# Kernel optimization log

Measured on AMD Instinct MI355X. Metric: run time of the kernel, lower is better.

The kernel has to match this reference:

```python
import jax, jax.numpy as jnp
import numpy as np

N_NODES = 100000
N_EDGES = 1000000
N_INPUT = 64
N_HIDDEN = 64
K = 8


def setup_inputs() -> dict:
    key = jax.random.key(0)
    k1, k2, k3, k4 = jax.random.split(key, 4)
    x = jax.random.normal(k1, (N_NODES, N_INPUT), dtype=jnp.float32)
    edge_index = jax.random.randint(k2, (2, N_EDGES), 0, N_NODES, dtype=jnp.int64)
    # ChebConv has K independent [in, out] weight matrices (Glorot-ish scale) and a bias.
    weight = jax.random.normal(k3, (K, N_INPUT, N_HIDDEN), dtype=jnp.float32) * (1.0 / np.sqrt(N_INPUT))
    bias = jax.random.normal(k4, (N_HIDDEN,), dtype=jnp.float32) * 0.01
    return {"x": x, "edge_index": edge_index, "weight": weight, "bias": bias}


def _cheb_edge_norm(edge_index, num_nodes):
    # PyG ChebConv sym normalization with default lambda_max=2.0:
    #   L_hat = (2/lambda_max) * (I - D^-1/2 A D^-1/2) - I = -D^-1/2 A D^-1/2
    # (the diagonal +1 from the Laplacian and the -1 self-loop cancel exactly).
    src, dst = edge_index[0], edge_index[1]
    ones = jnp.ones(src.shape[0], dtype=jnp.float32)
    deg = jax.ops.segment_sum(ones, src, num_segments=num_nodes)
    deg_inv_sqrt = jnp.where(deg > 0, jax.lax.rsqrt(jnp.maximum(deg, 1.0)), 0.0)
    return -deg_inv_sqrt[src] * deg_inv_sqrt[dst]  # [E]


def reference(x, edge_index, weight, bias):
    num_nodes = x.shape[0]
    src, dst = edge_index[0], edge_index[1]
    norm = _cheb_edge_norm(edge_index, num_nodes)

    def prop(h):  # h: [N, F] -> L_hat @ h via gather-multiply-scatter over edges
        return jax.ops.segment_sum(norm[:, None] * h[src], dst, num_segments=num_nodes)

    # Chebyshev recursion: T0 = x, T1 = L_hat x, Tk = 2 L_hat T_{k-1} - T_{k-2}
    Tx0 = x
    out = Tx0 @ weight[0]
    Tx1 = prop(Tx0)
    out = out + Tx1 @ weight[1]
    for k in range(2, weight.shape[0]):
        Tx2 = 2.0 * prop(Tx1) - Tx0
        out = out + Tx2 @ weight[k]
        Tx0, Tx1 = Tx1, Tx2
    out = out + bias
    # bn=False path: ReLU then dropout (identity in eval mode)
    return jax.nn.relu(out)
```

## Files before the change

### kernel.cpp

```cpp
#include <hip/hip_runtime.h>
#include <hip/hip_bf16.h>

typedef __attribute__((ext_vector_type(8))) short s16x8;
typedef __attribute__((ext_vector_type(4))) float f32x4;

#define HC 48
#define RBH 6400
#define RBS 3200

static __device__ __forceinline__ unsigned short f2bf(float f) {
    unsigned int u = __float_as_uint(f);
    unsigned int r = (u + 0x7FFFu + ((u >> 16) & 1u)) >> 16;
    return (unsigned short)r;
}

__global__ __launch_bounds__(256) void k_hist(const int* __restrict__ eidx,
                                              unsigned short* __restrict__ partials,
                                              int N, int E, int HR) {
    __shared__ int h[RBH];
    int b = blockIdx.x;
    int job = b / (HR * HC);
    int rc = b % (HR * HC);
    int r = rc / HC, c = rc % HC;
    int lo = r * RBH;
    int nb = min(RBH, N - lo);
    if (nb <= 0) return;
    for (int i = threadIdx.x; i < nb; i += 256) h[i] = 0;
    __syncthreads();
    const int* vals = eidx + (size_t)job * E;
    int e0 = (int)(((long long)E * c / HC) & ~3LL);
    int e1 = (c == HC - 1) ? E : (int)(((long long)E * (c + 1) / HC) & ~3LL);
    int e = e0 + threadIdx.x * 4;
    for (; e + 4 <= e1; e += 1024) {
        int4 v = *reinterpret_cast<const int4*>(vals + e);
        unsigned r0 = (unsigned)(v.x - lo), r1 = (unsigned)(v.y - lo);
        unsigned r2 = (unsigned)(v.z - lo), r3 = (unsigned)(v.w - lo);
        if (r0 < (unsigned)nb) atomicAdd(&h[r0], 1);
        if (r1 < (unsigned)nb) atomicAdd(&h[r1], 1);
        if (r2 < (unsigned)nb) atomicAdd(&h[r2], 1);
        if (r3 < (unsigned)nb) atomicAdd(&h[r3], 1);
    }
    if (threadIdx.x == 0)
        for (int t = e1 & ~3; t < e1; ++t) {
            unsigned rel = (unsigned)(vals[t] - lo);
            if (rel < (unsigned)nb) atomicAdd(&h[rel], 1);
        }
    __syncthreads();
    unsigned short* outp = partials + ((size_t)(job * HC + c)) * N + lo;
    for (int i = threadIdx.x; i < nb; i += 256) outp[i] = (unsigned short)h[i];
}

__global__ __launch_bounds__(1024) void k_rs(const unsigned short* __restrict__ partials,
                                             float* __restrict__ dis,
                                             float* __restrict__ dsi,
                                             int* __restrict__ cnt,
                                             int* __restrict__ incl,
                                             int* __restrict__ bsum, int N) {
    __shared__ int sm[1024];
    int t = threadIdx.x;
    int i = blockIdx.x * 1024 + t;
    int csum = 0;
    if (i < N) {
        int dsum = 0;
        for (int c = 0; c < HC; ++c) {
            dsum += partials[(size_t)c * N + i];
            csum += partials[(size_t)(HC + c) * N + i];
        }
        dis[i] = dsum > 0 ? rsqrtf((float)dsum) : 0.f;
        dsi[i] = dsum > 0 ? sqrtf((float)dsum) : 0.f;
        cnt[i] = csum;
    }
    sm[t] = (i < N) ? csum : 0;
    __syncthreads();
    for (int off = 1; off < 1024; off <<= 1) {
        int add = (t >= off) ? sm[t - off] : 0;
        __syncthreads();
        sm[t] += add;
        __syncthreads();
    }
    if (i < N) incl[i] = sm[t];
    if (t == 1023) bsum[blockIdx.x] = sm[1023];
}

__global__ __launch_bounds__(1024) void k_scan3(const int* __restrict__ cnt,
                                                const int* __restrict__ bsum,
                                                int* __restrict__ rowptr,
                                                const unsigned short* __restrict__ pdst,
                                                int* __restrict__ cbase, int N, int nb) {
    __shared__ int sb[128];
    int t = threadIdx.x;
    if (t < 128) sb[t] = (t < nb) ? bsum[t] : 0;
    __syncthreads();
    for (int off = 1; off < 128; off <<= 1) {
        int add = (t < 128 && t >= off) ? sb[t - off] : 0;
        __syncthreads();
        if (t < 128) sb[t] += add;
        __syncthreads();
    }
    int b = blockIdx.x;
    int boff = (b == 0) ? 0 : sb[b - 1];
    int total = sb[nb - 1];
    int i = b * 1024 + t;
    if (i >= N) return;
    int ex = rowptr[i] - cnt[i] + boff;
    rowptr[i] = ex;
    if (i == N - 1) rowptr[N] = total;
    int run = ex;
    for (int c = 0; c < HC; ++c) {
        size_t idx = (size_t)c * N + i;
        cbase[idx] = run;
        run += pdst[idx];
    }
}

__global__ __launch_bounds__(256) void k_scatter(
        const int* __restrict__ src, const int* __restrict__ dst,
        const int* __restrict__ cbase, int* __restrict__ srcs, int N, int E) {
    __shared__ int cur[RBS];
    int r = blockIdx.x / HC, c = blockIdx.x % HC;
    int lo = r * RBS;
    int nb = min(RBS, N - lo);
    if (nb <= 0) return;
    for (int i = threadIdx.x; i < nb; i += 256)
        cur[i] = cbase[(size_t)c * N + lo + i];
    __syncthreads();
    int e0 = (int)(((long long)E * c / HC) & ~3LL);
    int e1 = (c == HC - 1) ? E : (int)(((long long)E * (c + 1) / HC) & ~3LL);
    int e = e0 + threadIdx.x * 4;
    for (; e + 4 <= e1; e += 1024) {
        int4 d4 = *reinterpret_cast<const int4*>(dst + e);
        unsigned r0 = (unsigned)(d4.x - lo), r1 = (unsigned)(d4.y - lo);
        unsigned r2 = (unsigned)(d4.z - lo), r3 = (unsigned)(d4.w - lo);
        if (r0 < (unsigned)nb) srcs[atomicAdd(&cur[r0], 1)] = src[e];
        if (r1 < (unsigned)nb) srcs[atomicAdd(&cur[r1], 1)] = src[e + 1];
        if (r2 < (unsigned)nb) srcs[atomicAdd(&cur[r2], 1)] = src[e + 2];
        if (r3 < (unsigned)nb) srcs[atomicAdd(&cur[r3], 1)] = src[e + 3];
    }
    if (threadIdx.x == 0)
        for (int t = e1 & ~3; t < e1; ++t) {
            unsigned rel = (unsigned)(dst[t] - lo);
            if (rel < (unsigned)nb) srcs[atomicAdd(&cur[rel], 1)] = src[t];
        }
}

__global__ void k_pack(const float* __restrict__ x, const float* __restrict__ dis,
                       const float* __restrict__ W,
                       unsigned short* __restrict__ ysb, unsigned short* __restrict__ wt,
                       float* __restrict__ walt,
                       int N, int K, int PSE) {
    int t = blockIdx.x * blockDim.x + threadIdx.x;
    int nys = (N + 1) * 32;
    if (t < nys) {
        int row = t >> 5, p = t & 31;
        if (row == N) {
            for (int k = 0; k < K; ++k)
                *(unsigned*)(ysb + (size_t)k * PSE + ((size_t)N << 6) + (p << 1)) = 0;
            return;
        }
        size_t o = ((size_t)row << 6) + (p << 1);
        float2 v = *reinterpret_cast<const float2*>(x + o);
        float dv = dis[row];
        *(unsigned*)(ysb + o) = (unsigned)f2bf(v.x * dv) | ((unsigned)f2bf(v.y * dv) << 16);
    } else {
        int u = t - nys;
        if (u < K * 4096) {
            float v = W[u];
            int k = u >> 12;
            int r = u & 4095;
            int i = r >> 6;
            int j = r & 63;
            wt[(size_t)j * (K * 64) + (k << 6) + i] = f2bf(v);
        } else if (u < K * 4096 + 4096) {
            int u2 = u - K * 4096;
            float s = 0.f;
            for (int k = 0; k < K; k += 2)
                s += ((k & 3) == 0 ? 1.f : -1.f) * W[k * 4096 + u2];
            walt[u2] = s;
        }
    }
}

static __device__ __forceinline__ void addrow(float* acc, uint4 t) {
    acc[0] += __uint_as_float(t.x << 16);
    acc[1] += __uint_as_float(t.x & 0xffff0000u);
    acc[2] += __uint_as_float(t.y << 16);
    acc[3] += __uint_as_float(t.y & 0xffff0000u);
    acc[4] += __uint_as_float(t.z << 16);
    acc[5] += __uint_as_float(t.z & 0xffff0000u);
    acc[6] += __uint_as_float(t.w << 16);
    acc[7] += __uint_as_float(t.w & 0xffff0000u);
}

__global__ __launch_bounds__(256) void k_prop(
        const unsigned short* __restrict__ Ysin,
        const unsigned short* __restrict__ Ysm2,
        unsigned short* __restrict__ Ysout,
        const int* __restrict__ rowptr, const int* __restrict__ srcs,
        const float* __restrict__ dis,
        int N, int E, float scale, float beta) {
    int gt = blockIdx.x * blockDim.x + threadIdx.x;
    int wave0 = (gt >> 6) << 3;
    int lane = gt & 63;
    int g = lane >> 3;
    int i = lane & 7;
    int node = wave0 + g;
    bool live = node < N;
    int rs = 0, deg = 0;
    if (live) {
        rs = rowptr[node];
        deg = rowptr[node + 1] - rs;
    }
    int wmax = deg;
#pragma unroll
    for (int m = 8; m <= 32; m <<= 1) {
        int o = __shfl_xor(wmax, m);
        wmax = o > wmax ? o : wmax;
    }
    float acc[8];
#pragma unroll
    for (int j = 0; j < 8; ++j) acc[j] = 0.f;
    for (int e = 0; e < wmax; e += 8) {
        int b = rs + e;
        int s[8];
#pragma unroll
        for (int q = 0; q < 8; ++q)
            s[q] = (e + q < deg) ? srcs[min(b + q, E - 1)] : N;
        uint4 t[8];
#pragma unroll
        for (int q = 0; q < 8; ++q)
            t[q] = *reinterpret_cast<const uint4*>(Ysin + ((size_t)s[q] << 6) + (i << 3));
#pragma unroll
        for (int q = 0; q < 8; ++q) addrow(acc, t[q]);
    }
    if (live) {
        float dv = dis[node];
        float sc = -scale * dv * dv;
        size_t base = ((size_t)node << 6) + (i << 3);
        float r[8];
#pragma unroll
        for (int j = 0; j < 8; ++j) r[j] = sc * acc[j];
        if (beta != 0.f) {
            uint4 pv = *reinterpret_cast<const uint4*>(Ysm2 + base);
            r[0] = fmaf(beta, __uint_as_float(pv.x << 16), r[0]);
            r[1] = fmaf(beta, __uint_as_float(pv.x & 0xffff0000u), r[1]);
            r[2] = fmaf(beta, __uint_as_float(pv.y << 16), r[2]);
            r[3] = fmaf(beta, __uint_as_float(pv.y & 0xffff0000u), r[3]);
            r[4] = fmaf(beta, __uint_as_float(pv.z << 16), r[4]);
            r[5] = fmaf(beta, __uint_as_float(pv.z & 0xffff0000u), r[5]);
            r[6] = fmaf(beta, __uint_as_float(pv.w << 16), r[6]);
            r[7] = fmaf(beta, __uint_as_float(pv.w & 0xffff0000u), r[7]);
        }
        uint4 ov;
        ov.x = (unsigned)f2bf(r[0]) | ((unsigned)f2bf(r[1]) << 16);
        ov.y = (unsigned)f2bf(r[2]) | ((unsigned)f2bf(r[3]) << 16);
        ov.z = (unsigned)f2bf(r[4]) | ((unsigned)f2bf(r[5]) << 16);
        ov.w = (unsigned)f2bf(r[6]) | ((unsigned)f2bf(r[7]) << 16);
        *reinterpret_cast<uint4*>(Ysout + base) = ov;
    }
}

template <int KS>
__global__ __launch_bounds__(256) void k_gemm(const unsigned short* __restrict__ tb,
                                              const unsigned short* __restrict__ wt,
                                              const float* __restrict__ bias,
                                              const float* __restrict__ dsi,
                                              const float* __restrict__ x,
                                              const float* __restrict__ walt,
                                              float* __restrict__ out,
                                              int N, int PSE) {
    constexpr int NB = KS / 2;
    __shared__ unsigned short lds_b[KS * 512];
    __shared__ unsigned short lds_a[KS * 256 * 8];
    int tid = threadIdx.x;
    int lane = tid & 63;
    int w = tid >> 6;
    int l16 = lane & 15;
    int quad = lane >> 4;
    const int KI = KS * 32;

    {
        const unsigned short* wrow = wt + (size_t)(w * 16 + l16) * KI + quad * 8;
#pragma unroll
        for (int ks = 0; ks < KS; ++ks) {
            s16x8 v = *reinterpret_cast<const s16x8*>(wrow + ks * 32);
            *reinterpret_cast<s16x8*>(lds_a + (ks * 256 + tid) * 8) = v;
        }
    }
    f32x4 bias4 = *reinterpret_cast<const f32x4*>(bias + w * 16 + quad * 4);

    int ntiles = N >> 4;
    for (int t = blockIdx.x; t < ntiles; t += gridDim.x) {
        const char* tilebase = (const char*)tb + (size_t)t * 2048;
#pragma unroll
        for (int inst = 0; inst < 2 * NB; ++inst) {
            if ((inst & 3) != w) continue;
            int kbuf = inst >> 1;
            int j = inst & 1;
            int p = j * 64 + lane;
            int nrow = p >> 3;
            int s = (p & 7) ^ (nrow & 7);
            const char* g = tilebase + (size_t)kbuf * PSE * 2 + nrow * 128 + s * 16;
            __builtin_amdgcn_global_load_lds(
                (const __attribute__((address_space(1))) unsigned int*)g,
                (__attribute__((address_space(3))) unsigned int*)(lds_b + inst * 512),
                16, 0, 0);
        }
        __syncthreads();
        f32x4 acc = {0.f, 0.f, 0.f, 0.f};
#pragma unroll
        for (int ks = 0; ks < KS; ++ks) {
            s16x8 af = *reinterpret_cast<const s16x8*>(lds_a + (ks * 256 + tid) * 8);
            int kbuf = ks >> 1, half = ks & 1;
            int sph = (half * 4 + quad) ^ (l16 & 7);
            s16x8 bf = *reinterpret_cast<const s16x8*>(
                lds_b + kbuf * 1024 + l16 * 64 + sph * 8);
            acc = __builtin_amdgcn_mfma_f32_16x16x32_bf16(af, bf, acc, 0, 0, 0);
        }
        int row = t * 16 + l16;
        float dvi = dsi[row];
        float* orow = out + (size_t)row * 64 + w * 16 + quad * 4;
        f32x4 r;
        if (dvi != 0.f) {
#pragma unroll
            for (int q = 0; q < 4; ++q) {
                float v = fmaf(acc[q], dvi, bias4[q]);
                r[q] = v > 0.f ? v : 0.f;
            }
        } else {
            const float* xr = x + (size_t)row * 64;
            float rr[4] = {bias4[0], bias4[1], bias4[2], bias4[3]};
            for (int j = 0; j < 64; ++j) {
                float xv = xr[j];
                const float* wr = walt + j * 64 + w * 16 + quad * 4;
#pragma unroll
                for (int q = 0; q < 4; ++q) rr[q] = fmaf(xv, wr[q], rr[q]);
            }
#pragma unroll
            for (int q = 0; q < 4; ++q) r[q] = rr[q] > 0.f ? rr[q] : 0.f;
        }
        *reinterpret_cast<f32x4*>(orow) = r;
        __syncthreads();
    }
}

extern "C" void kernel_launch(void* const* d_in, const int* in_sizes, int n_in,
                              void* d_out, int out_size, void* d_ws, size_t ws_size,
                              hipStream_t stream) {
    const float* x    = (const float*)d_in[0];
    const int*   eidx = (const int*)d_in[1];
    const float* W    = (const float*)d_in[2];
    const float* bias = (const float*)d_in[3];
    float* out = (float*)d_out;

    const int NF = in_sizes[0];
    const int N  = NF / 64;
    const int E  = in_sizes[1] / 2;
    const int K  = in_sizes[2] / 4096;

    const int* src = eidx;
    const int* dst = eidx + E;

    const int PSE = (N + 1) * 64;

    char* ws = (char*)d_ws;
    size_t off = 0;
    auto alloc = [&](size_t bytes) -> char* {
        char* p = ws + off;
        off = (off + bytes + 255) & ~(size_t)255;
        return p;
    };
    unsigned short* Ysb = (unsigned short*)alloc((size_t)K * PSE * 2);
    unsigned short* Wt = (unsigned short*)alloc((size_t)64 * K * 64 * 2);
    float* Walt  = (float*)alloc(4096 * 4);
    int*   srcs   = (int*)alloc((size_t)E * 4);
    int*   rowptr = (int*)alloc((size_t)(N + 1) * 4);
    int*   cnt    = (int*)alloc((size_t)N * 4);
    unsigned short* partials = (unsigned short*)alloc((size_t)2 * HC * N * 2);
    int*   cbase  = (int*)alloc((size_t)HC * N * 4);
    float* dis  = (float*)alloc((size_t)N * 4);
    float* dsi  = (float*)alloc((size_t)N * 4);
    int*   bsum = (int*)alloc(1024);
    (void)ws_size; (void)n_in; (void)out_size;

    int HR = (N + RBH - 1) / RBH;
    int SR = (N + RBS - 1) / RBS;
    const unsigned short* pdst = partials + (size_t)HC * N;

    k_hist<<<2 * HR * HC, 256, 0, stream>>>(eidx, partials, N, E, HR);
    int nb = (N + 1023) / 1024;
    k_rs<<<nb, 1024, 0, stream>>>(partials, dis, dsi, cnt, rowptr, bsum, N);
    k_scan3<<<nb, 1024, 0, stream>>>(cnt, bsum, rowptr, pdst, cbase, N, nb);
    k_scatter<<<SR * HC, 256, 0, stream>>>(src, dst, cbase, srcs, N, E);
    int packn = (N + 1) * 32 + K * 4096 + 4096;
    k_pack<<<(packn + 255) / 256, 256, 0, stream>>>(x, dis, W, Ysb, Wt, Walt, N, K, PSE);

    int waves = (N + 7) / 8;
    int pblocks = (waves * 64 + 255) / 256;
    for (int p = 1; p < K; ++p) {
        float scale = (p == 1) ? 1.f : 2.f;
        float beta  = (p == 1) ? 0.f : -1.f;
        const unsigned short* Ysin = Ysb + (size_t)(p - 1) * PSE;
        const unsigned short* Ysm2 = Ysb + (size_t)(p >= 2 ? p - 2 : 0) * PSE;
        k_prop<<<pblocks, 256, 0, stream>>>(
            Ysin, Ysm2, Ysb + (size_t)p * PSE,
            rowptr, srcs, dis, N, E, scale, beta);
    }

    if (K == 8)      k_gemm<16><<<512, 256, 0, stream>>>(Ysb, Wt, bias, dsi, x, Walt, out, N, PSE);
    else if (K == 4) k_gemm<8><<<512, 256, 0, stream>>>(Ysb, Wt, bias, dsi, x, Walt, out, N, PSE);
    else if (K == 2) k_gemm<4><<<512, 256, 0, stream>>>(Ysb, Wt, bias, dsi, x, Walt, out, N, PSE);
    else if (K == 1) k_gemm<2><<<512, 256, 0, stream>>>(Ysb, Wt, bias, dsi, x, Walt, out, N, PSE);
}
```

Baseline: 324.9 us.

## Pack histogram counters as 16-bit pairs, double bucket ranges, fuse scatter with pack

The degree histogram now keeps two 16-bit counters in each 32-bit shared word, so each block covers twice as many nodes in the same shared memory. The scatter range is doubled as well, which halves the number of passes over the edge list in both kernels. The scatter and pack kernels are merged into a single launch that splits blocks by index, removing one launch and letting the two kinds of work overlap. The cost is more contention on shared atomics and a larger shared footprint in scatter (25.6KB), which may lower occupancy. A 16-bit counter overflows if one chunk holds more than 65535 edges for a single node.

```diff
diff --git a/kernel.cpp b/kernel.cpp
--- a/kernel.cpp
+++ b/kernel.cpp
@@ -5,8 +5,8 @@
 typedef __attribute__((ext_vector_type(4))) float f32x4;
 
 #define HC 48
-#define RBH 6400
-#define RBS 3200
+#define RBH 12800
+#define RBS 6400
 
 static __device__ __forceinline__ unsigned short f2bf(float f) {
     unsigned int u = __float_as_uint(f);
@@ -17,7 +17,7 @@
 __global__ __launch_bounds__(256) void k_hist(const int* __restrict__ eidx,
                                               unsigned short* __restrict__ partials,
                                               int N, int E, int HR) {
-    __shared__ int h[RBH];
+    __shared__ unsigned int h[RBH / 2];
     int b = blockIdx.x;
     int job = b / (HR * HC);
     int rc = b % (HR * HC);
@@ -25,7 +25,8 @@
     int lo = r * RBH;
     int nb = min(RBH, N - lo);
     if (nb <= 0) return;
-    for (int i = threadIdx.x; i < nb; i += 256) h[i] = 0;
+    int nw = (nb + 1) >> 1;
+    for (int i = threadIdx.x; i < nw; i += 256) h[i] = 0;
     __syncthreads();
     const int* vals = eidx + (size_t)job * E;
     int e0 = (int)(((long long)E * c / HC) & ~3LL);
@@ -35,19 +36,20 @@
         int4 v = *reinterpret_cast<const int4*>(vals + e);
         unsigned r0 = (unsigned)(v.x - lo), r1 = (unsigned)(v.y - lo);
         unsigned r2 = (unsigned)(v.z - lo), r3 = (unsigned)(v.w - lo);
-        if (r0 < (unsigned)nb) atomicAdd(&h[r0], 1);
-        if (r1 < (unsigned)nb) atomicAdd(&h[r1], 1);
-        if (r2 < (unsigned)nb) atomicAdd(&h[r2], 1);
-        if (r3 < (unsigned)nb) atomicAdd(&h[r3], 1);
+        if (r0 < (unsigned)nb) atomicAdd(&h[r0 >> 1], 1u << ((r0 & 1) << 4));
+        if (r1 < (unsigned)nb) atomicAdd(&h[r1 >> 1], 1u << ((r1 & 1) << 4));
+        if (r2 < (unsigned)nb) atomicAdd(&h[r2 >> 1], 1u << ((r2 & 1) << 4));
+        if (r3 < (unsigned)nb) atomicAdd(&h[r3 >> 1], 1u << ((r3 & 1) << 4));
     }
     if (threadIdx.x == 0)
         for (int t = e1 & ~3; t < e1; ++t) {
             unsigned rel = (unsigned)(vals[t] - lo);
-            if (rel < (unsigned)nb) atomicAdd(&h[rel], 1);
+            if (rel < (unsigned)nb) atomicAdd(&h[rel >> 1], 1u << ((rel & 1) << 4));
         }
     __syncthreads();
     unsigned short* outp = partials + ((size_t)(job * HC + c)) * N + lo;
-    for (int i = threadIdx.x; i < nb; i += 256) outp[i] = (unsigned short)h[i];
+    for (int i = threadIdx.x; i < nb; i += 256)
+        outp[i] = (unsigned short)((h[i >> 1] >> ((i & 1) << 4)) & 0xffffu);
 }
 
 __global__ __launch_bounds__(1024) void k_rs(const unsigned short* __restrict__ partials,
@@ -113,69 +115,69 @@
     }
 }
 
-__global__ __launch_bounds__(256) void k_scatter(
+__global__ __launch_bounds__(256) void k_scpk(
         const int* __restrict__ src, const int* __restrict__ dst,
-        const int* __restrict__ cbase, int* __restrict__ srcs, int N, int E) {
+        const int* __restrict__ cbase, int* __restrict__ srcs, int N, int E, int SB,
+        const float* __restrict__ x, const float* __restrict__ dis,
+        const float* __restrict__ W,
+        unsigned short* __restrict__ ysb, unsigned short* __restrict__ wt,
+        float* __restrict__ walt, int K, int PSE) {
     __shared__ int cur[RBS];
-    int r = blockIdx.x / HC, c = blockIdx.x % HC;
-    int lo = r * RBS;
-    int nb = min(RBS, N - lo);
-    if (nb <= 0) return;
-    for (int i = threadIdx.x; i < nb; i += 256)
-        cur[i] = cbase[(size_t)c * N + lo + i];
-    __syncthreads();
-    int e0 = (int)(((long long)E * c / HC) & ~3LL);
-    int e1 = (c == HC - 1) ? E : (int)(((long long)E * (c + 1) / HC) & ~3LL);
-    int e = e0 + threadIdx.x * 4;
-    for (; e + 4 <= e1; e += 1024) {
-        int4 d4 = *reinterpret_cast<const int4*>(dst + e);
-        unsigned r0 = (unsigned)(d4.x - lo), r1 = (unsigned)(d4.y - lo);
-        unsigned r2 = (unsigned)(d4.z - lo), r3 = (unsigned)(d4.w - lo);
-        if (r0 < (unsigned)nb) srcs[atomicAdd(&cur[r0], 1)] = src[e];
-        if (r1 < (unsigned)nb) srcs[atomicAdd(&cur[r1], 1)] = src[e + 1];
-        if (r2 < (unsigned)nb) srcs[atomicAdd(&cur[r2], 1)] = src[e + 2];
-        if (r3 < (unsigned)nb) srcs[atomicAdd(&cur[r3], 1)] = src[e + 3];
-    }
-    if (threadIdx.x == 0)
-        for (int t = e1 & ~3; t < e1; ++t) {
-            unsigned rel = (unsigned)(dst[t] - lo);
-            if (rel < (unsigned)nb) srcs[atomicAdd(&cur[rel], 1)] = src[t];
-        }
-}
-
-__global__ void k_pack(const float* __restrict__ x, const float* __restrict__ dis,
-                       const float* __restrict__ W,
-                       unsigned short* __restrict__ ysb, unsigned short* __restrict__ wt,
-                       float* __restrict__ walt,
-                       int N, int K, int PSE) {
-    int t = blockIdx.x * blockDim.x + threadIdx.x;
-    int nys = (N + 1) * 32;
-    if (t < nys) {
-        int row = t >> 5, p = t & 31;
-        if (row == N) {
-            for (int k = 0; k < K; ++k)
-                *(unsigned*)(ysb + (size_t)k * PSE + ((size_t)N << 6) + (p << 1)) = 0;
-            return;
-        }
-        size_t o = ((size_t)row << 6) + (p << 1);
-        float2 v = *reinterpret_cast<const float2*>(x + o);
-        float dv = dis[row];
-        *(unsigned*)(ysb + o) = (unsigned)f2bf(v.x * dv) | ((unsigned)f2bf(v.y * dv) << 16);
+    if ((int)blockIdx.x < SB) {
+        int r = blockIdx.x / HC, c = blockIdx.x % HC;
+        int lo = r * RBS;
+        int nb = min(RBS, N - lo);
+        if (nb <= 0) return;
+        for (int i = threadIdx.x; i < nb; i += 256)
+            cur[i] = cbase[(size_t)c * N + lo + i];
+        __syncthreads();
+        int e0 = (int)(((long long)E * c / HC) & ~3LL);
+        int e1 = (c == HC - 1) ? E : (int)(((long long)E * (c + 1) / HC) & ~3LL);
+        int e = e0 + threadIdx.x * 4;
+        for (; e + 4 <= e1; e += 1024) {
+            int4 d4 = *reinterpret_cast<const int4*>(dst + e);
+            unsigned r0 = (unsigned)(d4.x - lo), r1 = (unsigned)(d4.y - lo);
+            unsigned r2 = (unsigned)(d4.z - lo), r3 = (unsigned)(d4.w - lo);
+            if (r0 < (unsigned)nb) srcs[atomicAdd(&cur[r0], 1)] = src[e];
+            if (r1 < (unsigned)nb) srcs[atomicAdd(&cur[r1], 1)] = src[e + 1];
+            if (r2 < (unsigned)nb) srcs[atomicAdd(&cur[r2], 1)] = src[e + 2];
+            if (r3 < (unsigned)nb) srcs[atomicAdd(&cur[r3], 1)] = src[e + 3];
+        }
+        if (threadIdx.x == 0)
+            for (int t = e1 & ~3; t < e1; ++t) {
+                unsigned rel = (unsigned)(dst[t] - lo);
+                if (rel < (unsigned)nb) srcs[atomicAdd(&cur[rel], 1)] = src[t];
+            }
     } else {
-        int u = t - nys;
-        if (u < K * 4096) {
-            float v = W[u];
-            int k = u >> 12;
-            int r = u & 4095;
-            int i = r >> 6;
-            int j = r & 63;
-            wt[(size_t)j * (K * 64) + (k << 6) + i] = f2bf(v);
-        } else if (u < K * 4096 + 4096) {
-            int u2 = u - K * 4096;
-            float s = 0.f;
-            for (int k = 0; k < K; k += 2)
-                s += ((k & 3) == 0 ? 1.f : -1.f) * W[k * 4096 + u2];
-            walt[u2] = s;
+        int t = (blockIdx.x - SB) * 256 + threadIdx.x;
+        int nys = (N + 1) * 32;
+        if (t < nys) {
+            int row = t >> 5, p = t & 31;
+            if (row == N) {
+                for (int k = 0; k < K; ++k)
+                    *(unsigned*)(ysb + (size_t)k * PSE + ((size_t)N << 6) + (p << 1)) = 0;
+                return;
+            }
+            size_t o = ((size_t)row << 6) + (p << 1);
+            float2 v = *reinterpret_cast<const float2*>(x + o);
+            float dv = dis[row];
+            *(unsigned*)(ysb + o) = (unsigned)f2bf(v.x * dv) | ((unsigned)f2bf(v.y * dv) << 16);
+        } else {
+            int u = t - nys;
+            if (u < K * 4096) {
+                float v = W[u];
+                int k = u >> 12;
+                int r = u & 4095;
+                int i = r >> 6;
+                int j = r & 63;
+                wt[(size_t)j * (K * 64) + (k << 6) + i] = f2bf(v);
+            } else if (u < K * 4096 + 4096) {
+                int u2 = u - K * 4096;
+                float s = 0.f;
+                for (int k = 0; k < K; k += 2)
+                    s += ((k & 3) == 0 ? 1.f : -1.f) * W[k * 4096 + u2];
+                walt[u2] = s;
+            }
         }
     }
 }
@@ -390,9 +392,12 @@
     int nb = (N + 1023) / 1024;
     k_rs<<<nb, 1024, 0, stream>>>(partials, dis, dsi, cnt, rowptr, bsum, N);
     k_scan3<<<nb, 1024, 0, stream>>>(cnt, bsum, rowptr, pdst, cbase, N, nb);
-    k_scatter<<<SR * HC, 256, 0, stream>>>(src, dst, cbase, srcs, N, E);
+
+    int SB = SR * HC;
     int packn = (N + 1) * 32 + K * 4096 + 4096;
-    k_pack<<<(packn + 255) / 256, 256, 0, stream>>>(x, dis, W, Ysb, Wt, Walt, N, K, PSE);
+    int pblk = (packn + 255) / 256;
+    k_scpk<<<SB + pblk, 256, 0, stream>>>(src, dst, cbase, srcs, N, E, SB,
+                                          x, dis, W, Ysb, Wt, Walt, K, PSE);
 
     int waves = (N + 7) / 8;
     int pblocks = (waves * 64 + 255) / 256;
```

After: 317.4 us (median of 2 runs). -2.3%, faster.
